# Kernel optimization log

Hardware: AMD Instinct MI355X
Metric: run time of the kernel (lower is better)

The kernel has to match this reference:

```python
import jax, jax.numpy as jnp
import numpy as np

N_EDGE_TYPE = 7
BN_EPS = 1e-5


def setup_inputs() -> dict:
    key = jax.random.key(0)
    k1, k2, k3, k4, k5 = jax.random.split(key, 5)
    N, C_in, C_out, E = 100000, 128, 128, 700000
    x = jax.random.normal(k1, (N, C_in), dtype=jnp.float32)
    row = jax.random.randint(k2, (E,), 0, N, dtype=jnp.int64)
    col = jax.random.randint(k3, (E,), 0, N, dtype=jnp.int64)
    edge_type = jax.random.randint(k4, (E,), 0, N_EDGE_TYPE, dtype=jnp.int64)
    # init like torch: uniform(-a, a), a = sqrt(3)*sqrt(2/(7*C_in + 7*C_out))
    a = np.sqrt(3.0) * np.sqrt(2.0 / float(7 * C_in + 7 * C_out))
    weights = jax.random.uniform(k5, (N_EDGE_TYPE * C_in, C_out), dtype=jnp.float32, minval=-a, maxval=a)
    gamma = jnp.ones((C_out,), dtype=jnp.float32)
    beta = jnp.zeros((C_out,), dtype=jnp.float32)
    return {"x": x, "row": row, "col": col, "edge_type": edge_type,
            "weights": weights, "gamma": gamma, "beta": beta}


def reference(x, row, col, edge_type, weights, gamma, beta):
    N, C = x.shape
    n_seg = N * N_EDGE_TYPE
    idx = row * N_EDGE_TYPE + edge_type  # [E]
    # scatter_mean of x[col] into [N*n_edge_type, C]
    sums = jax.ops.segment_sum(x[col], idx, num_segments=n_seg)  # [7N, C]
    cnt = jax.ops.segment_sum(jnp.ones_like(idx, dtype=x.dtype), idx, num_segments=n_seg)
    col_data = sums / jnp.maximum(cnt, 1.0)[:, None]
    # overwrite the last edge-type slot with the node's own features
    self_idx = jnp.arange(N, dtype=jnp.int64) * N_EDGE_TYPE + (N_EDGE_TYPE - 1)
    col_data = col_data.at[self_idx].set(x)
    # dense matmul: [N, 7*C] @ [7*C, C_out]
    out = col_data.reshape(N, N_EDGE_TYPE * C) @ weights
    # BatchNorm1d (training mode: batch statistics, biased variance)
    mean = jnp.mean(out, axis=0)
    var = jnp.mean(jnp.square(out - mean), axis=0)
    out = (out - mean) * jax.lax.rsqrt(var + BN_EPS) * gamma + beta
    return out
```

## Files before the change

kernel.cpp:

```cpp
#include <hip/hip_runtime.h>
#include <hip/hip_bf16.h>


typedef float  f32x4  __attribute__((ext_vector_type(4)));
typedef short  short8 __attribute__((ext_vector_type(8)));
typedef __bf16 bf16x8 __attribute__((ext_vector_type(8)));

union BFrag { uint4 q; short8 s; bf16x8 b; unsigned int u[4]; };

__device__ inline unsigned short f2bfbits(float f) {
    union { float f; unsigned int u; } v; v.f = f;
    unsigned int u = v.u;
    u += 0x7fffu + ((u >> 16) & 1u);
    return (unsigned short)(u >> 16);
}
__device__ inline unsigned int pk_bf16(float lo, float hi) {
    float2 f; f.x = lo; f.y = hi;
    union { __hip_bfloat162 h; unsigned int u; } v;
    v.h = __float22bfloat162_rn(f);
    return v.u;
}
__device__ inline float bflo(unsigned int p) {
    union { unsigned int u; float f; } v; v.u = p << 16; return v.f;
}
__device__ inline float bfhi(unsigned int p) {
    union { unsigned int u; float f; } v; v.u = p & 0xffff0000u; return v.f;
}

#define BUCKET_CAP 31
#define ROWW 32
#define LROW 452
#define TNODES 16
#define NPX 1024

__device__ inline int idx_at(const int* __restrict__ p, int e, int mode) {
    return p[mode ? (e << 1) : e];
}

__global__ __launch_bounds__(256) void prep_k(
    const float* __restrict__ x, const int* __restrict__ row,
    const int* __restrict__ col, const int* __restrict__ et,
    const float* __restrict__ w,
    unsigned int* __restrict__ xbu, short8* __restrict__ wp,
    unsigned int* __restrict__ meta, unsigned int* __restrict__ ovfcnt,
    int* __restrict__ ovf, int* __restrict__ novf,
    int E, int N, int nEB)
{
    const int bid = blockIdx.x;
    const int tid = threadIdx.x;

    if (bid < nEB) {
        const int li = tid & 63;
        int vodd = (li < 32) ? row[2 * li + 1] : 0;
        const int mode = __any(vodd != 0) ? 0 : 1;

        const int e = bid * 256 + tid;
        if (e < E) {
            int r = idx_at(row, e, mode);
            int c = idx_at(col, e, mode);
            int t = idx_at(et,  e, mode);
            if ((unsigned)r < (unsigned)N && (unsigned)c < (unsigned)N &&
                (unsigned)t < 6u) {
                unsigned pos = atomicAdd(&meta[(size_t)r * ROWW], 1u);
                if (pos < BUCKET_CAP) {
                    meta[(size_t)r * ROWW + 1 + pos] = (unsigned)((c << 3) | t);
                } else {
                    atomicAdd(&ovfcnt[r * 7 + t], 1u);
                    ovf[atomicAdd(novf, 1)] = e;
                }
            }
        }
    } else if (bid < nEB + NPX) {
        const size_t total4 = (size_t)N * 32;
        for (size_t v = (size_t)(bid - nEB) * 256 + tid; v < total4;
             v += (size_t)NPX * 256) {
            f32x4 t = *(const f32x4*)(x + v * 4);
            xbu[v * 2]     = pk_bf16(t[0], t[1]);
            xbu[v * 2 + 1] = pk_bf16(t[2], t[3]);
        }
    } else {
        int u = (bid - nEB - NPX) * 256 + tid;
        if (u < 7 * 8 * 4 * 64) {
            int lane = u & 63, kc = (u >> 6) & 3, nt = (u >> 8) & 7, t = u >> 11;
            int quad = lane >> 4, lr = lane & 15;
            short8 s;
#pragma unroll
            for (int j = 0; j < 8; ++j)
                s[j] = (short)f2bfbits(
                    w[(size_t)(t * 128 + kc * 32 + quad * 8 + j) * 128
                      + nt * 16 + lr]);
            wp[u] = s;
        }
    }
}

__global__ __launch_bounds__(512, 8) void fused_k(
    const unsigned int* __restrict__ meta, const unsigned int* __restrict__ ovfcnt,
    const unsigned int* __restrict__ xbu, const uint4* __restrict__ wpq,
    float* __restrict__ out, float* __restrict__ statsR, int N)
{
    __shared__ unsigned int cold[TNODES * LROW];
    const int tid  = threadIdx.x;
    const int l    = tid & 63;
    const int wv   = tid >> 6;
    const int quad = l >> 4, lr = l & 15;
    const int tile = blockIdx.x * TNODES;
    const int base = tile + wv * 2;

    unsigned mv = 0, self = 0;
    if (base < N) {
        mv   = (l < ROWW) ? meta[(size_t)base * ROWW + l] : 0u;
        self = xbu[(size_t)base * 64 + l];
    }
#pragma unroll
    for (int i = 0; i < 2; ++i) {
        const int r = base + i;
        if (r < N) {
            const unsigned fl = __shfl(mv, 0);
            const int nE = __builtin_amdgcn_readfirstlane(
                               (int)min(fl, (unsigned)BUCKET_CAP));
            const unsigned sv   = self;
            const unsigned mcur = mv;

            float acc[6][2];
#pragma unroll
            for (int t = 0; t < 6; ++t) { acc[t][0] = 0.f; acc[t][1] = 0.f; }

            unsigned q[8]; int pj[8];
            if (nE > 0) {
#pragma unroll
                for (int j = 0; j < 8; ++j) {
                    pj[j] = (int)__shfl(mcur, 1 + min(j, nE - 1));
                    q[j]  = xbu[(size_t)(pj[j] >> 3) * 64 + l];
                }
            }
            if (i == 0 && r + 1 < N) {
                mv   = (l < ROWW) ? meta[(size_t)(r + 1) * ROWW + l] : 0u;
                self = xbu[(size_t)(r + 1) * 64 + l];
            }
            if (nE > 0) {
#pragma unroll
                for (int j = 0; j < 8; ++j) {
                    unsigned qq = (j < nE) ? q[j] : 0u;
                    float lo = bflo(qq), hi = bfhi(qq);
                    switch (__builtin_amdgcn_readfirstlane(pj[j] & 7)) {
                        case 0: acc[0][0] += lo; acc[0][1] += hi; break;
                        case 1: acc[1][0] += lo; acc[1][1] += hi; break;
                        case 2: acc[2][0] += lo; acc[2][1] += hi; break;
                        case 3: acc[3][0] += lo; acc[3][1] += hi; break;
                        case 4: acc[4][0] += lo; acc[4][1] += hi; break;
                        default: acc[5][0] += lo; acc[5][1] += hi; break;
                    }
                }
                for (int k = 8; k < nE; k += 8) {
                    const int rem = nE - k;
#pragma unroll
                    for (int j = 0; j < 8; ++j) {
                        pj[j] = (int)__shfl(mcur, 1 + k + min(j, rem - 1));
                        q[j]  = xbu[(size_t)(pj[j] >> 3) * 64 + l];
                    }
#pragma unroll
                    for (int j = 0; j < 8; ++j) {
                        unsigned qq = (j < rem) ? q[j] : 0u;
                        float lo = bflo(qq), hi = bfhi(qq);
                        switch (__builtin_amdgcn_readfirstlane(pj[j] & 7)) {
                            case 0: acc[0][0] += lo; acc[0][1] += hi; break;
                            case 1: acc[1][0] += lo; acc[1][1] += hi; break;
                            case 2: acc[2][0] += lo; acc[2][1] += hi; break;
                            case 3: acc[3][0] += lo; acc[3][1] += hi; break;
                            case 4: acc[4][0] += lo; acc[4][1] += hi; break;
                            default: acc[5][0] += lo; acc[5][1] += hi; break;
                        }
                    }
                }
            }

            const bool inb = (l >= 1) && (l < 1 + nE);
            int c0 = (int)__popcll(__ballot(inb && ((mcur & 7u) == 0u)));
            int c1 = (int)__popcll(__ballot(inb && ((mcur & 7u) == 1u)));
            int c2 = (int)__popcll(__ballot(inb && ((mcur & 7u) == 2u)));
            int c3 = (int)__popcll(__ballot(inb && ((mcur & 7u) == 3u)));
            int c4 = (int)__popcll(__ballot(inb && ((mcur & 7u) == 4u)));
            int c5 = (int)__popcll(__ballot(inb && ((mcur & 7u) == 5u)));
            if (fl > (unsigned)BUCKET_CAP) {
                c0 += (int)ovfcnt[r * 7 + 0]; c1 += (int)ovfcnt[r * 7 + 1];
                c2 += (int)ovfcnt[r * 7 + 2]; c3 += (int)ovfcnt[r * 7 + 3];
                c4 += (int)ovfcnt[r * 7 + 4]; c5 += (int)ovfcnt[r * 7 + 5];
            }
            const float iv0 = 1.0f / (float)max(c0, 1);
            const float iv1 = 1.0f / (float)max(c1, 1);
            const float iv2 = 1.0f / (float)max(c2, 1);
            const float iv3 = 1.0f / (float)max(c3, 1);
            const float iv4 = 1.0f / (float)max(c4, 1);
            const float iv5 = 1.0f / (float)max(c5, 1);

            const int mrow = (wv * 2 + i) * LROW;
            cold[mrow + 0 * 64 + l] = pk_bf16(acc[0][0] * iv0, acc[0][1] * iv0);
            cold[mrow + 1 * 64 + l] = pk_bf16(acc[1][0] * iv1, acc[1][1] * iv1);
            cold[mrow + 2 * 64 + l] = pk_bf16(acc[2][0] * iv2, acc[2][1] * iv2);
            cold[mrow + 3 * 64 + l] = pk_bf16(acc[3][0] * iv3, acc[3][1] * iv3);
            cold[mrow + 4 * 64 + l] = pk_bf16(acc[4][0] * iv4, acc[4][1] * iv4);
            cold[mrow + 5 * 64 + l] = pk_bf16(acc[5][0] * iv5, acc[5][1] * iv5);
            cold[mrow + 6 * 64 + l] = sv;
        }
    }
    __syncthreads();

    f32x4 oa0 = (f32x4){0.f, 0.f, 0.f, 0.f};
    f32x4 oa1 = (f32x4){0.f, 0.f, 0.f, 0.f};
#pragma unroll
    for (int t = 0; t < 4; ++t)
#pragma unroll
        for (int kc = 0; kc < 4; ++kc) {
            BFrag a, b;
            const int ko = t * 64 + kc * 16 + quad * 4;
            a.q = *(const uint4*)&cold[lr * LROW + ko];
            b.q = wpq[(size_t)(((t * 8 + wv) * 4 + kc) * 64) + l];
            oa0 = __builtin_amdgcn_mfma_f32_16x16x32_bf16(a.b, b.b, oa0, 0, 0, 0);
        }
#pragma unroll
    for (int t = 4; t < 7; ++t)
#pragma unroll
        for (int kc = 0; kc < 4; ++kc) {
            BFrag a, b;
            const int ko = t * 64 + kc * 16 + quad * 4;
            a.q = *(const uint4*)&cold[lr * LROW + ko];
            b.q = wpq[(size_t)(((t * 8 + wv) * 4 + kc) * 64) + l];
            oa1 = __builtin_amdgcn_mfma_f32_16x16x32_bf16(a.b, b.b, oa1, 0, 0, 0);
        }
    float s = 0.f, s2 = 0.f;
    const int ch = wv * 16 + lr;
#pragma unroll
    for (int j = 0; j < 4; ++j) {
        int m = tile + quad * 4 + j;
        if (m < N) {
            float v = oa0[j] + oa1[j];
            out[(size_t)m * 128 + ch] = v;
            s += v; s2 += v * v;
        }
    }
    s  += __shfl_xor(s, 16);  s  += __shfl_xor(s, 32);
    s2 += __shfl_xor(s2, 16); s2 += __shfl_xor(s2, 32);
    if (l < 16) {
        float* st = statsR + (size_t)(blockIdx.x & 7) * 256;
        atomicAdd(&st[ch],       s);
        atomicAdd(&st[128 + ch], s2);
    }
}

__global__ void ovf_k(const int* __restrict__ ovf, const int* __restrict__ novf,
                      const int* __restrict__ row, const int* __restrict__ col,
                      const int* __restrict__ et,
                      const unsigned int* __restrict__ xbu,
                      const unsigned int* __restrict__ meta,
                      const unsigned int* __restrict__ ovfcnt,
                      const float* __restrict__ w,
                      float* __restrict__ out, float* __restrict__ statsR,
                      int nwaves)
{
    const int n = novf[0];
    if (n == 0) return;
    int s = 0;
#pragma unroll
    for (int i = 1; i < 64; i += 2) s |= row[i];
    const int mode = (s == 0) ? 1 : 0;
    const int l = threadIdx.x & 63;
    for (int i = (blockIdx.x * 256 + threadIdx.x) >> 6; i < n; i += nwaves) {
        int e = ovf[i];
        int r = idx_at(row, e, mode);
        int c = idx_at(col, e, mode);
        int t = idx_at(et,  e, mode);
        unsigned mv = (l < ROWW) ? meta[(size_t)r * ROWW + l] : 0u;
        unsigned fl = __shfl(mv, 0);
        int nE = (int)min(fl, (unsigned)BUCKET_CAP);
        bool inb = (l >= 1) && (l < 1 + nE);
        int ct = (int)__popcll(__ballot(inb && ((int)(mv & 7u) == t)))
               + (int)ovfcnt[r * 7 + t];
        float inv = 1.0f / (float)max(ct, 1);
        float d0 = 0.f, d1 = 0.f;
        for (int k = 0; k < 64; ++k) {
            unsigned xv = xbu[(size_t)c * 64 + k];
            float xlo = bflo(xv), xhi = bfhi(xv);
            const float* wr = w + (size_t)(t * 128 + 2 * k) * 128;
            d0 += xlo * wr[2 * l]     + xhi * wr[128 + 2 * l];
            d1 += xlo * wr[2 * l + 1] + xhi * wr[128 + 2 * l + 1];
        }
        d0 *= inv; d1 *= inv;
        float olo = atomicAdd(&out[(size_t)r * 128 + 2 * l],     d0);
        float ohi = atomicAdd(&out[(size_t)r * 128 + 2 * l + 1], d1);
        atomicAdd(&statsR[2 * l],           d0);
        atomicAdd(&statsR[128 + 2 * l],     d0 * (2.f * olo + d0));
        atomicAdd(&statsR[2 * l + 1],       d1);
        atomicAdd(&statsR[128 + 2 * l + 1], d1 * (2.f * ohi + d1));
    }
}

__global__ __launch_bounds__(256) void norm_k(
    float* __restrict__ out, const float* __restrict__ statsR,
    const float* __restrict__ gamma, const float* __restrict__ beta, int N)
{
    const int c0 = (threadIdx.x * 4) & 127;
    const float invN = 1.0f / (float)N;
    f32x4 sc, bi;
#pragma unroll
    for (int j = 0; j < 4; ++j) {
        int c = c0 + j;
        float sm = 0.f, sq = 0.f;
#pragma unroll
        for (int rep = 0; rep < 8; ++rep) {
            sm += statsR[rep * 256 + c];
            sq += statsR[rep * 256 + 128 + c];
        }
        float mean = sm * invN;
        float var  = sq * invN - mean * mean;
        float s = gamma[c] * rsqrtf(var + 1e-5f);
        sc[j] = s; bi[j] = beta[c] - mean * s;
    }
    const size_t nv = (size_t)N * 32;
    for (size_t v = (size_t)blockIdx.x * 256 + threadIdx.x; v < nv;
         v += (size_t)gridDim.x * 256) {
        f32x4 x = *(f32x4*)(out + v * 4);
#pragma unroll
        for (int j = 0; j < 4; ++j) x[j] = x[j] * sc[j] + bi[j];
        *(f32x4*)(out + v * 4) = x;
    }
}

extern "C" void kernel_launch(void* const* d_in, const int* in_sizes, int n_in,
                              void* d_out, int out_size, void* d_ws, size_t ws_size,
                              hipStream_t stream)
{
    const float* x     = (const float*)d_in[0];
    const int*   row   = (const int*)d_in[1];
    const int*   col   = (const int*)d_in[2];
    const int*   etype = (const int*)d_in[3];
    const float* w     = (const float*)d_in[4];
    const float* gamma = (const float*)d_in[5];
    const float* beta  = (const float*)d_in[6];
    float* out = (float*)d_out;

    const int N = in_sizes[0] / 128;
    const int E = in_sizes[1];

    char* ws = (char*)d_ws;
    unsigned int* xbu    = (unsigned int*)ws;
    short8*       wp     = (short8*)(ws + (size_t)N * 256);
    unsigned int* meta   = (unsigned int*)((char*)wp + 7 * 8 * 4 * 64 * 16);
    unsigned int* ovfcnt = (unsigned int*)((char*)meta + (size_t)N * ROWW * 4);
    int*          ovf    = (int*)((char*)ovfcnt + (size_t)N * 7 * 4);
    float*        stats  = (float*)((char*)ovf + (size_t)E * 4);
    int*          novf   = (int*)((char*)stats + 8 * 256 * 4);

    hipMemsetAsync(meta,   0, (size_t)N * ROWW * 4, stream);
    hipMemsetAsync(ovfcnt, 0, (size_t)N * 7 * 4,    stream);
    hipMemsetAsync(stats,  0, 8 * 256 * 4 + 8,      stream);

    const int nEB = (E + 255) / 256;
    const int nPW = (7 * 8 * 4 * 64 + 255) / 256;
    prep_k<<<nEB + NPX + nPW, 256, 0, stream>>>(x, row, col, etype, w,
                                                xbu, wp, meta, ovfcnt,
                                                ovf, novf, E, N, nEB);
    fused_k<<<(N + TNODES - 1) / TNODES, 512, 0, stream>>>(meta, ovfcnt, xbu,
                                                           (const uint4*)wp, out,
                                                           stats, N);
    ovf_k<<<64, 256, 0, stream>>>(ovf, novf, row, col, etype,
                                  xbu, meta, ovfcnt, w, out, stats, 256);
    norm_k<<<2048, 256, 0, stream>>>(out, stats, gamma, beta, N);
}
```

Baseline: 256.0 us.

## Replace fixed-capacity row buckets with histogram, block-allocated offsets and compact edge buffer

The fixed 32-slot per-row bucket array with overflow list is replaced by a three-pass build: a per-row count histogram, a block-level scan that hands out unordered base offsets through a global atomic counter, and a scatter into a compact edge buffer. The fused kernel reads each row's count and base offset, loads up to 64 edges per wave and walks any remainder serially, so the separate overflow kernel goes away. This cuts the large zero-fill memset and the per-row meta footprint, but adds two kernel launches and a second pass over the edge arrays.

Measured after the change: 285.4 us. 11.5% more time.

```diff
diff --git a/kernel.cpp b/kernel.cpp
--- a/kernel.cpp
+++ b/kernel.cpp
@@ -27,8 +27,6 @@
     union { unsigned int u; float f; } v; v.u = p & 0xffff0000u; return v.f;
 }
 
-#define BUCKET_CAP 31
-#define ROWW 32
 #define LROW 452
 #define TNODES 16
 #define NPX 1024
@@ -36,39 +34,32 @@
 __device__ inline int idx_at(const int* __restrict__ p, int e, int mode) {
     return p[mode ? (e << 1) : e];
 }
-
-__global__ __launch_bounds__(256) void prep_k(
+__device__ inline int detect_mode(const int* __restrict__ row, int tid) {
+    const int li = tid & 63;
+    int vodd = (li < 32) ? row[2 * li + 1] : 0;
+    return __any(vodd != 0) ? 0 : 1;
+}
+
+__global__ __launch_bounds__(256) void hist_k(
     const float* __restrict__ x, const int* __restrict__ row,
     const int* __restrict__ col, const int* __restrict__ et,
     const float* __restrict__ w,
     unsigned int* __restrict__ xbu, short8* __restrict__ wp,
-    unsigned int* __restrict__ meta, unsigned int* __restrict__ ovfcnt,
-    int* __restrict__ ovf, int* __restrict__ novf,
-    int E, int N, int nEB)
+    unsigned int* __restrict__ cnt, int E, int N, int nEB)
 {
     const int bid = blockIdx.x;
     const int tid = threadIdx.x;
 
     if (bid < nEB) {
-        const int li = tid & 63;
-        int vodd = (li < 32) ? row[2 * li + 1] : 0;
-        const int mode = __any(vodd != 0) ? 0 : 1;
-
+        const int mode = detect_mode(row, tid);
         const int e = bid * 256 + tid;
         if (e < E) {
             int r = idx_at(row, e, mode);
             int c = idx_at(col, e, mode);
             int t = idx_at(et,  e, mode);
             if ((unsigned)r < (unsigned)N && (unsigned)c < (unsigned)N &&
-                (unsigned)t < 6u) {
-                unsigned pos = atomicAdd(&meta[(size_t)r * ROWW], 1u);
-                if (pos < BUCKET_CAP) {
-                    meta[(size_t)r * ROWW + 1 + pos] = (unsigned)((c << 3) | t);
-                } else {
-                    atomicAdd(&ovfcnt[r * 7 + t], 1u);
-                    ovf[atomicAdd(novf, 1)] = e;
-                }
-            }
+                (unsigned)t < 6u)
+                atomicAdd(&cnt[r], 1u);
         }
     } else if (bid < nEB + NPX) {
         const size_t total4 = (size_t)N * 32;
@@ -94,10 +85,57 @@
     }
 }
 
+__global__ __launch_bounds__(256) void alloc_k(const unsigned int* __restrict__ cnt,
+                                               unsigned int* __restrict__ basep,
+                                               unsigned int* __restrict__ gctr,
+                                               int N)
+{
+    const int i = blockIdx.x * 256 + threadIdx.x;
+    const int l = threadIdx.x & 63;
+    const int wv = threadIdx.x >> 6;
+    unsigned c = (i < N) ? cnt[i] : 0u;
+    unsigned s = c;
+#pragma unroll
+    for (int d = 1; d < 64; d <<= 1) {
+        unsigned t = __shfl_up(s, d);
+        if (l >= d) s += t;
+    }
+    __shared__ unsigned wt[4], wb[4];
+    if (l == 63) wt[wv] = s;
+    __syncthreads();
+    if (threadIdx.x == 0) {
+        unsigned tot = wt[0] + wt[1] + wt[2] + wt[3];
+        unsigned gb  = atomicAdd(gctr, tot);
+        unsigned run = gb;
+#pragma unroll
+        for (int k = 0; k < 4; ++k) { wb[k] = run; run += wt[k]; }
+    }
+    __syncthreads();
+    if (i < N) basep[i] = wb[wv] + s - c;
+}
+
+__global__ __launch_bounds__(256) void scat_k(
+    const int* __restrict__ row, const int* __restrict__ col,
+    const int* __restrict__ et, unsigned int* __restrict__ basep,
+    int* __restrict__ ebuf, int E, int N)
+{
+    const int mode = detect_mode(row, threadIdx.x);
+    const int e = blockIdx.x * 256 + threadIdx.x;
+    if (e >= E) return;
+    int r = idx_at(row, e, mode);
+    int c = idx_at(col, e, mode);
+    int t = idx_at(et,  e, mode);
+    if ((unsigned)r < (unsigned)N && (unsigned)c < (unsigned)N && (unsigned)t < 6u) {
+        unsigned pos = atomicAdd(&basep[r], 1u);
+        ebuf[pos] = (c << 3) | t;
+    }
+}
+
 __global__ __launch_bounds__(512, 8) void fused_k(
-    const unsigned int* __restrict__ meta, const unsigned int* __restrict__ ovfcnt,
-    const unsigned int* __restrict__ xbu, const uint4* __restrict__ wpq,
-    float* __restrict__ out, float* __restrict__ statsR, int N)
+    const unsigned int* __restrict__ cnt, const unsigned int* __restrict__ basep,
+    const int* __restrict__ ebuf, const unsigned int* __restrict__ xbu,
+    const uint4* __restrict__ wpq, float* __restrict__ out,
+    float* __restrict__ statsR, int N)
 {
     __shared__ unsigned int cold[TNODES * LROW];
     const int tid  = threadIdx.x;
@@ -105,43 +143,53 @@
     const int wv   = tid >> 6;
     const int quad = l >> 4, lr = l & 15;
     const int tile = blockIdx.x * TNODES;
-    const int base = tile + wv * 2;
-
-    unsigned mv = 0, self = 0;
-    if (base < N) {
-        mv   = (l < ROWW) ? meta[(size_t)base * ROWW + l] : 0u;
-        self = xbu[(size_t)base * 64 + l];
-    }
+    const int node0 = tile + wv * 2;
+
+    unsigned cb = 0;
+    if (node0 < N) {
+        int rr = node0 + (l >> 1);
+        if (l < 4 && rr < N) cb = (l & 1) ? basep[rr] : cnt[rr];
+    }
+    unsigned nEa[2], sta[2], paya[2], selfa[2];
+    nEa[0] = (unsigned)__builtin_amdgcn_readlane((int)cb, 0);
+    sta[0] = (unsigned)__builtin_amdgcn_readlane((int)cb, 1) - nEa[0];
+    nEa[1] = (unsigned)__builtin_amdgcn_readlane((int)cb, 2);
+    sta[1] = (unsigned)__builtin_amdgcn_readlane((int)cb, 3) - nEa[1];
+    paya[0] = paya[1] = 0u; selfa[0] = selfa[1] = 0u;
+    if (node0 < N) {
+        if (l < (int)min(nEa[0], 64u)) paya[0] = (unsigned)ebuf[sta[0] + l];
+        selfa[0] = xbu[(size_t)node0 * 64 + l];
+        if (node0 + 1 < N) {
+            if (l < (int)min(nEa[1], 64u)) paya[1] = (unsigned)ebuf[sta[1] + l];
+            selfa[1] = xbu[(size_t)(node0 + 1) * 64 + l];
+        }
+    }
+
 #pragma unroll
     for (int i = 0; i < 2; ++i) {
-        const int r = base + i;
+        const int r = node0 + i;
         if (r < N) {
-            const unsigned fl = __shfl(mv, 0);
-            const int nE = __builtin_amdgcn_readfirstlane(
-                               (int)min(fl, (unsigned)BUCKET_CAP));
-            const unsigned sv   = self;
-            const unsigned mcur = mv;
+            const unsigned nEf  = nEa[i];
+            const int      nE   = __builtin_amdgcn_readfirstlane(
+                                      (int)min(nEf, 64u));
+            const unsigned mcur = paya[i];
+            const unsigned sv   = selfa[i];
 
             float acc[6][2];
 #pragma unroll
             for (int t = 0; t < 6; ++t) { acc[t][0] = 0.f; acc[t][1] = 0.f; }
 
             unsigned q[8]; int pj[8];
-            if (nE > 0) {
+            for (int k = 0; k < nE; k += 8) {
+                const int rem = nE - k;
 #pragma unroll
                 for (int j = 0; j < 8; ++j) {
-                    pj[j] = (int)__shfl(mcur, 1 + min(j, nE - 1));
+                    pj[j] = (int)__shfl(mcur, k + min(j, rem - 1));
                     q[j]  = xbu[(size_t)(pj[j] >> 3) * 64 + l];
                 }
-            }
-            if (i == 0 && r + 1 < N) {
-                mv   = (l < ROWW) ? meta[(size_t)(r + 1) * ROWW + l] : 0u;
-                self = xbu[(size_t)(r + 1) * 64 + l];
-            }
-            if (nE > 0) {
 #pragma unroll
                 for (int j = 0; j < 8; ++j) {
-                    unsigned qq = (j < nE) ? q[j] : 0u;
+                    unsigned qq = (j < rem) ? q[j] : 0u;
                     float lo = bflo(qq), hi = bfhi(qq);
                     switch (__builtin_amdgcn_readfirstlane(pj[j] & 7)) {
                         case 0: acc[0][0] += lo; acc[0][1] += hi; break;
@@ -152,41 +200,30 @@
                         default: acc[5][0] += lo; acc[5][1] += hi; break;
                     }
                 }
-                for (int k = 8; k < nE; k += 8) {
-                    const int rem = nE - k;
-#pragma unroll
-                    for (int j = 0; j < 8; ++j) {
-                        pj[j] = (int)__shfl(mcur, 1 + k + min(j, rem - 1));
-                        q[j]  = xbu[(size_t)(pj[j] >> 3) * 64 + l];
-                    }
-#pragma unroll
-                    for (int j = 0; j < 8; ++j) {
-                        unsigned qq = (j < rem) ? q[j] : 0u;
-                        float lo = bflo(qq), hi = bfhi(qq);
-                        switch (__builtin_amdgcn_readfirstlane(pj[j] & 7)) {
-                            case 0: acc[0][0] += lo; acc[0][1] += hi; break;
-                            case 1: acc[1][0] += lo; acc[1][1] += hi; break;
-                            case 2: acc[2][0] += lo; acc[2][1] += hi; break;
-                            case 3: acc[3][0] += lo; acc[3][1] += hi; break;
-                            case 4: acc[4][0] += lo; acc[4][1] += hi; break;
-                            default: acc[5][0] += lo; acc[5][1] += hi; break;
-                        }
-                    }
-                }
             }
 
-            const bool inb = (l >= 1) && (l < 1 + nE);
+            const bool inb = l < nE;
             int c0 = (int)__popcll(__ballot(inb && ((mcur & 7u) == 0u)));
             int c1 = (int)__popcll(__ballot(inb && ((mcur & 7u) == 1u)));
             int c2 = (int)__popcll(__ballot(inb && ((mcur & 7u) == 2u)));
             int c3 = (int)__popcll(__ballot(inb && ((mcur & 7u) == 3u)));
             int c4 = (int)__popcll(__ballot(inb && ((mcur & 7u) == 4u)));
             int c5 = (int)__popcll(__ballot(inb && ((mcur & 7u) == 5u)));
-            if (fl > (unsigned)BUCKET_CAP) {
-                c0 += (int)ovfcnt[r * 7 + 0]; c1 += (int)ovfcnt[r * 7 + 1];
-                c2 += (int)ovfcnt[r * 7 + 2]; c3 += (int)ovfcnt[r * 7 + 3];
-                c4 += (int)ovfcnt[r * 7 + 4]; c5 += (int)ovfcnt[r * 7 + 5];
+
+            for (unsigned k = 64u; k < nEf; ++k) {
+                int p = ebuf[sta[i] + k];
+                unsigned qv = xbu[(size_t)(p >> 3) * 64 + l];
+                float lo = bflo(qv), hi = bfhi(qv);
+                switch (__builtin_amdgcn_readfirstlane(p & 7)) {
+                    case 0: acc[0][0] += lo; acc[0][1] += hi; ++c0; break;
+                    case 1: acc[1][0] += lo; acc[1][1] += hi; ++c1; break;
+                    case 2: acc[2][0] += lo; acc[2][1] += hi; ++c2; break;
+                    case 3: acc[3][0] += lo; acc[3][1] += hi; ++c3; break;
+                    case 4: acc[4][0] += lo; acc[4][1] += hi; ++c4; break;
+                    default: acc[5][0] += lo; acc[5][1] += hi; ++c5; break;
+                }
             }
+
             const float iv0 = 1.0f / (float)max(c0, 1);
             const float iv1 = 1.0f / (float)max(c1, 1);
             const float iv2 = 1.0f / (float)max(c2, 1);
@@ -248,53 +285,6 @@
     }
 }
 
-__global__ void ovf_k(const int* __restrict__ ovf, const int* __restrict__ novf,
-                      const int* __restrict__ row, const int* __restrict__ col,
-                      const int* __restrict__ et,
-                      const unsigned int* __restrict__ xbu,
-                      const unsigned int* __restrict__ meta,
-                      const unsigned int* __restrict__ ovfcnt,
-                      const float* __restrict__ w,
-                      float* __restrict__ out, float* __restrict__ statsR,
-                      int nwaves)
-{
-    const int n = novf[0];
-    if (n == 0) return;
-    int s = 0;
-#pragma unroll
-    for (int i = 1; i < 64; i += 2) s |= row[i];
-    const int mode = (s == 0) ? 1 : 0;
-    const int l = threadIdx.x & 63;
-    for (int i = (blockIdx.x * 256 + threadIdx.x) >> 6; i < n; i += nwaves) {
-        int e = ovf[i];
-        int r = idx_at(row, e, mode);
-        int c = idx_at(col, e, mode);
-        int t = idx_at(et,  e, mode);
-        unsigned mv = (l < ROWW) ? meta[(size_t)r * ROWW + l] : 0u;
-        unsigned fl = __shfl(mv, 0);
-        int nE = (int)min(fl, (unsigned)BUCKET_CAP);
-        bool inb = (l >= 1) && (l < 1 + nE);
-        int ct = (int)__popcll(__ballot(inb && ((int)(mv & 7u) == t)))
-               + (int)ovfcnt[r * 7 + t];
-        float inv = 1.0f / (float)max(ct, 1);
-        float d0 = 0.f, d1 = 0.f;
-        for (int k = 0; k < 64; ++k) {
-            unsigned xv = xbu[(size_t)c * 64 + k];
-            float xlo = bflo(xv), xhi = bfhi(xv);
-            const float* wr = w + (size_t)(t * 128 + 2 * k) * 128;
-            d0 += xlo * wr[2 * l]     + xhi * wr[128 + 2 * l];
-            d1 += xlo * wr[2 * l + 1] + xhi * wr[128 + 2 * l + 1];
-        }
-        d0 *= inv; d1 *= inv;
-        float olo = atomicAdd(&out[(size_t)r * 128 + 2 * l],     d0);
-        float ohi = atomicAdd(&out[(size_t)r * 128 + 2 * l + 1], d1);
-        atomicAdd(&statsR[2 * l],           d0);
-        atomicAdd(&statsR[128 + 2 * l],     d0 * (2.f * olo + d0));
-        atomicAdd(&statsR[2 * l + 1],       d1);
-        atomicAdd(&statsR[128 + 2 * l + 1], d1 * (2.f * ohi + d1));
-    }
-}
-
 __global__ __launch_bounds__(256) void norm_k(
     float* __restrict__ out, const float* __restrict__ statsR,
     const float* __restrict__ gamma, const float* __restrict__ beta, int N)
@@ -343,27 +333,25 @@
     const int E = in_sizes[1];
 
     char* ws = (char*)d_ws;
-    unsigned int* xbu    = (unsigned int*)ws;
-    short8*       wp     = (short8*)(ws + (size_t)N * 256);
-    unsigned int* meta   = (unsigned int*)((char*)wp + 7 * 8 * 4 * 64 * 16);
-    unsigned int* ovfcnt = (unsigned int*)((char*)meta + (size_t)N * ROWW * 4);
-    int*          ovf    = (int*)((char*)ovfcnt + (size_t)N * 7 * 4);
-    float*        stats  = (float*)((char*)ovf + (size_t)E * 4);
-    int*          novf   = (int*)((char*)stats + 8 * 256 * 4);
-
-    hipMemsetAsync(meta,   0, (size_t)N * ROWW * 4, stream);
-    hipMemsetAsync(ovfcnt, 0, (size_t)N * 7 * 4,    stream);
-    hipMemsetAsync(stats,  0, 8 * 256 * 4 + 8,      stream);
+    unsigned int* xbu   = (unsigned int*)ws;
+    short8*       wp    = (short8*)(ws + (size_t)N * 256);
+    unsigned int* cnt   = (unsigned int*)((char*)wp + 7 * 8 * 4 * 64 * 16);
+    unsigned int* basep = cnt + N;
+    int*          ebuf  = (int*)(basep + N);
+    float*        stats = (float*)(ebuf + E);
+    unsigned int* gctr  = (unsigned int*)(stats + 8 * 256);
+
+    hipMemsetAsync(cnt,   0, (size_t)N * 4,        stream);
+    hipMemsetAsync(stats, 0, 8 * 256 * 4 + 8,      stream);
 
     const int nEB = (E + 255) / 256;
     const int nPW = (7 * 8 * 4 * 64 + 255) / 256;
-    prep_k<<<nEB + NPX + nPW, 256, 0, stream>>>(x, row, col, etype, w,
-                                                xbu, wp, meta, ovfcnt,
-                                                ovf, novf, E, N, nEB);
-    fused_k<<<(N + TNODES - 1) / TNODES, 512, 0, stream>>>(meta, ovfcnt, xbu,
+    hist_k<<<nEB + NPX + nPW, 256, 0, stream>>>(x, row, col, etype, w,
+                                                xbu, wp, cnt, E, N, nEB);
+    alloc_k<<<(N + 255) / 256, 256, 0, stream>>>(cnt, basep, gctr, N);
+    scat_k<<<nEB, 256, 0, stream>>>(row, col, etype, basep, ebuf, E, N);
+    fused_k<<<(N + TNODES - 1) / TNODES, 512, 0, stream>>>(cnt, basep, ebuf, xbu,
                                                            (const uint4*)wp, out,
                                                            stats, N);
-    ovf_k<<<64, 256, 0, stream>>>(ovf, novf, row, col, etype,
-                                  xbu, meta, ovfcnt, w, out, stats, 256);
     norm_k<<<2048, 256, 0, stream>>>(out, stats, gamma, beta, N);
 }
```
